# Kernel tuning notes

Measured on AMD Instinct MI355X. Metric: run time of the kernel, lower is better.

The kernel has to match this reference:

```python
import jax, jax.numpy as jnp
import numpy as np

N_NODES = 50000
N_EDGES = 800000
IN_CH = 128
HEADS = 4
HID = 32  # per-head dim; heads*hid = 128
N_GRAPHS = 128


def setup_inputs() -> dict:
    key = jax.random.key(0)
    ks = jax.random.split(key, 32)
    d = {}
    d["x"] = jax.random.normal(ks[0], (N_NODES, IN_CH), dtype=jnp.float32)
    d["edge_index"] = jax.random.randint(ks[1], (2, N_EDGES), 0, N_NODES, dtype=jnp.int64)
    d["batch"] = jnp.sort(jax.random.randint(ks[2], (N_NODES,), 0, N_GRAPHS, dtype=jnp.int64))
    HD = HEADS * HID
    names = [("wq1", (IN_CH, HD)), ("bq1", (HD,)), ("wk1", (IN_CH, HD)), ("bk1", (HD,)),
             ("wv1", (IN_CH, HD)), ("bv1", (HD,)), ("ws1", (IN_CH, HD)), ("bs1", (HD,)),
             ("wq2", (HD, HD)), ("bq2", (HD,)), ("wk2", (HD, HD)), ("bk2", (HD,)),
             ("wv2", (HD, HD)), ("bv2", (HD,)), ("ws2", (HD, HD)), ("bs2", (HD,)),
             ("wl", (HD, HD)), ("bl", (HD,)), ("wl2", (HD, 1)), ("bl2", (1,))]
    for i, (nm, shp) in enumerate(names):
        d[nm] = jax.random.normal(ks[3 + i], shp, dtype=jnp.float32) * 0.05
    return d


def _transformer_conv(x, src, dst, wq, bq, wk, bk, wv, bv, ws, bs):
    """PyG TransformerConv: multi-head dot-product attention over edges,
    softmax normalized per destination node, plus linear root/skip term."""
    N = x.shape[0]
    q = (x @ wq + bq).reshape(N, HEADS, HID)
    k = (x @ wk + bk).reshape(N, HEADS, HID)
    v = (x @ wv + bv).reshape(N, HEADS, HID)
    # edge scores: [E, H]
    e = jnp.einsum('ehd,ehd->eh', q[dst], k[src]) * np.float32(1.0 / np.sqrt(HID))
    # segment softmax over incoming edges of each destination node
    m = jax.ops.segment_max(e, dst, num_segments=N)
    a = jnp.exp(e - m[dst])
    s = jax.ops.segment_sum(a, dst, num_segments=N)
    alpha = a / s[dst]  # [E, H]
    msg = alpha[:, :, None] * v[src]  # [E, H, D]
    out = jax.ops.segment_sum(msg, dst, num_segments=N).reshape(N, HEADS * HID)
    return out + x @ ws + bs  # root weight (skip) term


def reference(x, edge_index, batch,
              wq1, bq1, wk1, bk1, wv1, bv1, ws1, bs1,
              wq2, bq2, wk2, bk2, wv2, bv2, ws2, bs2,
              wl, bl, wl2, bl2):
    src, dst = edge_index[0], edge_index[1]
    h = _transformer_conv(x, src, dst, wq1, bq1, wk1, bk1, wv1, bv1, ws1, bs1)
    h = jax.nn.relu(h)
    h = _transformer_conv(h, src, dst, wq2, bq2, wk2, bk2, wv2, bv2, ws2, bs2)
    h = jax.nn.relu(h)
    h = h @ wl + bl
    h = h @ wl2 + bl2  # [N, 1]
    # global mean pool over graphs
    sums = jax.ops.segment_sum(h, batch, num_segments=N_GRAPHS)
    cnts = jax.ops.segment_sum(jnp.ones((h.shape[0], 1), h.dtype), batch, num_segments=N_GRAPHS)
    return sums / jnp.maximum(cnts, 1.0)
```

## Files before the change

kernel.cpp:

```cpp
#include <hip/hip_runtime.h>
#include <hip/hip_bf16.h>
#include <math.h>

#define NNODES 50000
#define NEDGES 800000
#define NGRAPHS 128
#define SCAN_B ((NNODES + 255) / 256)

typedef __attribute__((ext_vector_type(8))) short bf16x8;
typedef __attribute__((ext_vector_type(4))) float f32x4;

__device__ __forceinline__ unsigned short f2bf(float f) {
    unsigned int u = __float_as_uint(f);
    return (unsigned short)((u + 0x7FFFu + ((u >> 16) & 1u)) >> 16);
}
__device__ __forceinline__ float2 bf2f2(unsigned int u) {
    float2 f;
    f.x = __uint_as_float(u << 16);
    f.y = __uint_as_float(u & 0xFFFF0000u);
    return f;
}

__global__ void count_edges(const int* __restrict__ ei, int* __restrict__ cnt) {
    int e = blockIdx.x * 256 + threadIdx.x;
    if (e < NEDGES) atomicAdd(&cnt[ei[NEDGES + e]], 1);
}

__global__ __launch_bounds__(256)
void scan_pass1(const int* __restrict__ cnt, int* __restrict__ bsum) {
    const int t = threadIdx.x;
    const int i = blockIdx.x * 256 + t;
    int v = (i < NNODES) ? cnt[i] : 0;
#pragma unroll
    for (int off = 32; off > 0; off >>= 1) v += __shfl_xor(v, off, 64);
    __shared__ int ws[4];
    if ((t & 63) == 0) ws[t >> 6] = v;
    __syncthreads();
    if (t == 0) bsum[blockIdx.x] = ws[0] + ws[1] + ws[2] + ws[3];
}

__global__ __launch_bounds__(256)
void scan_pass2(const int* __restrict__ bsum, int* __restrict__ boff) {
    const int t = threadIdx.x;
    const int v = (t < SCAN_B) ? bsum[t] : 0;
    __shared__ int a[256];
    a[t] = v;
    __syncthreads();
    for (int off = 1; off < 256; off <<= 1) {
        const int u = (t >= off) ? a[t - off] : 0;
        __syncthreads();
        a[t] += u;
        __syncthreads();
    }
    if (t < SCAN_B) boff[t] = a[t] - v;
}

__global__ __launch_bounds__(256)
void scan_pass3(const int* __restrict__ cnt, const int* __restrict__ boff,
                int* __restrict__ rowptr, int* __restrict__ wpos) {
    const int t = threadIdx.x;
    const int i = blockIdx.x * 256 + t;
    const int v = (i < NNODES) ? cnt[i] : 0;
    __shared__ int a[256];
    a[t] = v;
    __syncthreads();
    for (int off = 1; off < 256; off <<= 1) {
        const int u = (t >= off) ? a[t - off] : 0;
        __syncthreads();
        a[t] += u;
        __syncthreads();
    }
    if (i < NNODES) {
        const int e = boff[blockIdx.x] + a[t] - v;
        rowptr[i] = e;
        wpos[i]   = e;
    }
    if (i == 0) rowptr[NNODES] = NEDGES;
}

__global__ void fill_csr(const int* __restrict__ ei, int* __restrict__ wpos,
                         int* __restrict__ colsrc) {
    int e = blockIdx.x * 256 + threadIdx.x;
    if (e < NEDGES) {
        int d = ei[NEDGES + e];
        int slot = atomicAdd(&wpos[d], 1);
        colsrc[slot] = ei[e];
    }
}

__global__ void fuse_wl(const float* __restrict__ wl, const float* __restrict__ bl,
                        const float* __restrict__ wl2, const float* __restrict__ bl2,
                        float* __restrict__ wf, float* __restrict__ bf) {
    int t = threadIdx.x;
    float s = 0.f;
    for (int j = 0; j < 128; ++j) s += wl[t * 128 + j] * wl2[j];
    wf[t] = s;
    if (t == 0) {
        float s2 = 0.f;
        for (int j = 0; j < 128; ++j) s2 += bl[j] * wl2[j];
        bf[0] = s2 + bl2[0];
    }
}

__global__ void prep_w(const float* __restrict__ wq, const float* __restrict__ wk,
                       const float* __restrict__ wv, const float* __restrict__ wsk,
                       unsigned short* __restrict__ Wt) {
    const int sel = blockIdx.y;
    const float* W = sel == 0 ? wq : sel == 1 ? wk : sel == 2 ? wv : wsk;
    const int idx = blockIdx.x * 256 + threadIdx.x;
    const int col = idx & 127;
    const int k   = idx >> 7;
    Wt[sel * 16384 + col * 128 + k] = f2bf(W[k * 128 + col]);
}

__global__ __launch_bounds__(256)
void gemm_qkvs(const float* __restrict__ F, const unsigned short* __restrict__ Wt,
               const float* __restrict__ bq, const float* __restrict__ bk,
               const float* __restrict__ bv, const float* __restrict__ bsk,
               float* __restrict__ Q, unsigned short* __restrict__ Kb,
               unsigned short* __restrict__ Vb, float* __restrict__ H) {
    __shared__ __align__(16) unsigned short As[128][136];
    __shared__ __align__(16) unsigned short Bt[64][136];
    const int t    = threadIdx.x;
    const int m0   = blockIdx.x * 128;
    const int lane = t & 63;
    const int w    = t >> 6;
    const int l15  = lane & 15;
    const int lg   = lane >> 4;

    {
        const int row = t >> 1;
        const int kh  = (t & 1) * 64;
        const int gr  = min(m0 + row, NNODES - 1);
        const float* src = &F[(size_t)gr * 128 + kh];
#pragma unroll
        for (int p = 0; p < 16; ++p) {
            const float4 v = *(const float4*)&src[p * 4];
            ushort4 u;
            u.x = f2bf(v.x); u.y = f2bf(v.y); u.z = f2bf(v.z); u.w = f2bf(v.w);
            *(ushort4*)&As[row][kh + p * 4] = u;
        }
    }

    for (int sl = 0; sl < 8; ++sl) {
        const int sel = sl >> 1;
        const int c0  = (sl & 1) * 64;
        const float* bias = sel == 0 ? bq : sel == 1 ? bk : sel == 2 ? bv : bsk;

        {
            const int col = t >> 2;
            const int kb  = (t & 3) * 32;
            const unsigned short* src = &Wt[sel * 16384 + (c0 + col) * 128 + kb];
#pragma unroll
            for (int p = 0; p < 4; ++p)
                *(uint4*)&Bt[col][kb + p * 8] = *(const uint4*)&src[p * 8];
        }
        __syncthreads();

        const float b0 = bias[c0 + l15];
        const float b1 = bias[c0 + 16 + l15];
        const float b2 = bias[c0 + 32 + l15];
        const float b3 = bias[c0 + 48 + l15];
        f32x4 a00 = {b0, b0, b0, b0}, a01 = {b1, b1, b1, b1},
              a02 = {b2, b2, b2, b2}, a03 = {b3, b3, b3, b3};
        f32x4 a10 = a00, a11 = a01, a12 = a02, a13 = a03;
#pragma unroll
        for (int ks = 0; ks < 4; ++ks) {
            const int kof = ks * 32 + lg * 8;
            const bf16x8 af0 = *(const bf16x8*)&As[w * 32 + l15][kof];
            const bf16x8 af1 = *(const bf16x8*)&As[w * 32 + 16 + l15][kof];
            const bf16x8 bf0 = *(const bf16x8*)&Bt[l15][kof];
            const bf16x8 bf1 = *(const bf16x8*)&Bt[16 + l15][kof];
            const bf16x8 bf2 = *(const bf16x8*)&Bt[32 + l15][kof];
            const bf16x8 bf3 = *(const bf16x8*)&Bt[48 + l15][kof];
            a00 = __builtin_amdgcn_mfma_f32_16x16x32_bf16(af0, bf0, a00, 0, 0, 0);
            a01 = __builtin_amdgcn_mfma_f32_16x16x32_bf16(af0, bf1, a01, 0, 0, 0);
            a02 = __builtin_amdgcn_mfma_f32_16x16x32_bf16(af0, bf2, a02, 0, 0, 0);
            a03 = __builtin_amdgcn_mfma_f32_16x16x32_bf16(af0, bf3, a03, 0, 0, 0);
            a10 = __builtin_amdgcn_mfma_f32_16x16x32_bf16(af1, bf0, a10, 0, 0, 0);
            a11 = __builtin_amdgcn_mfma_f32_16x16x32_bf16(af1, bf1, a11, 0, 0, 0);
            a12 = __builtin_amdgcn_mfma_f32_16x16x32_bf16(af1, bf2, a12, 0, 0, 0);
            a13 = __builtin_amdgcn_mfma_f32_16x16x32_bf16(af1, bf3, a13, 0, 0, 0);
        }
        __syncthreads();

        const int r0 = m0 + w * 32 + lg * 4;
        if (sel == 1 || sel == 2) {
            unsigned short* Ob = sel == 1 ? Kb : Vb;
#define STB(ACC, RT, CT)                                                       \
            _Pragma("unroll")                                                  \
            for (int i = 0; i < 4; ++i) {                                      \
                const int gr = r0 + (RT) * 16 + i;                             \
                if (gr < NNODES)                                               \
                    Ob[(size_t)gr * 128 + c0 + (CT) * 16 + l15] = f2bf(ACC[i]);\
            }
            STB(a00, 0, 0) STB(a01, 0, 1) STB(a02, 0, 2) STB(a03, 0, 3)
            STB(a10, 1, 0) STB(a11, 1, 1) STB(a12, 1, 2) STB(a13, 1, 3)
#undef STB
        } else {
            float* O = sel == 0 ? Q : H;
#define ST(ACC, RT, CT)                                                        \
            _Pragma("unroll")                                                  \
            for (int i = 0; i < 4; ++i) {                                      \
                const int gr = r0 + (RT) * 16 + i;                             \
                if (gr < NNODES)                                               \
                    O[(size_t)gr * 128 + c0 + (CT) * 16 + l15] = ACC[i];       \
            }
            ST(a00, 0, 0) ST(a01, 0, 1) ST(a02, 0, 2) ST(a03, 0, 3)
            ST(a10, 1, 0) ST(a11, 1, 1) ST(a12, 1, 2) ST(a13, 1, 3)
#undef ST
        }
    }
}

template <bool FUSE_HEAD>
__global__ __launch_bounds__(128)
void attn_agg(const float* __restrict__ Q, const unsigned short* __restrict__ Kb,
              const unsigned short* __restrict__ Vb, float* __restrict__ H,
              const int* __restrict__ rowptr, const int* __restrict__ colsrc,
              const float* __restrict__ wf, float* __restrict__ r) {
    const int n    = blockIdx.x * 2 + (threadIdx.x >> 6);
    const int l    = threadIdx.x & 63;
    const int half = l >> 5;
    const int c    = (l & 31) * 4;
    const float4 q4 = *(const float4*)&Q[(size_t)n * 128 + c];
    const float sc_ = 0.17677669529663687f;
    const float q0 = q4.x * sc_, q1 = q4.y * sc_, q2 = q4.z * sc_, q3 = q4.w * sc_;
    const int beg = rowptr[n], end = rowptr[n + 1];
    const int cnt = end - beg;

    float m = -INFINITY, s = 0.f;
    float a0 = 0.f, a1 = 0.f, a2 = 0.f, a3 = 0.f;

    uint2 ku, vu;
    if (cnt > 0) {
        const int src = colsrc[min(beg + half, end - 1)];
        ku = *(const uint2*)&Kb[(size_t)src * 128 + c];
        vu = *(const uint2*)&Vb[(size_t)src * 128 + c];
    }
    for (int i = beg; i < end; i += 2) {
        const uint2 kc = ku, vc = vu;
        const bool valid = (i + half) < end;
        if (i + 2 < end) {
            const int srcN = colsrc[min(i + 2 + half, end - 1)];
            ku = *(const uint2*)&Kb[(size_t)srcN * 128 + c];
            vu = *(const uint2*)&Vb[(size_t)srcN * 128 + c];
        }
        const float2 k01 = bf2f2(kc.x), k23 = bf2f2(kc.y);
        float p = fmaf(q0, k01.x, fmaf(q1, k01.y, fmaf(q2, k23.x, q3 * k23.y)));
        p += __shfl_xor(p, 4);
        p += __shfl_xor(p, 2);
        p += __shfl_xor(p, 1);
        if (!valid) p = -INFINITY;
        const float pO = __shfl_xor(p, 32);
        const float nm = fmaxf(fmaxf(p, pO), m);
        const float sc = __expf(m - nm);
        const float w  = __expf(p - nm);
        s = fmaf(s, sc, w);
        const float2 v01 = bf2f2(vc.x), v23 = bf2f2(vc.y);
        a0 = fmaf(a0, sc, w * v01.x);
        a1 = fmaf(a1, sc, w * v01.y);
        a2 = fmaf(a2, sc, w * v23.x);
        a3 = fmaf(a3, sc, w * v23.y);
        m = nm;
    }
    s  += __shfl_xor(s, 32);
    a0 += __shfl_xor(a0, 32);
    a1 += __shfl_xor(a1, 32);
    a2 += __shfl_xor(a2, 32);
    a3 += __shfl_xor(a3, 32);

    const float4 hv = *(const float4*)&H[(size_t)n * 128 + c];
    float o0 = hv.x, o1 = hv.y, o2 = hv.z, o3 = hv.w;
    if (cnt > 0) {
        const float inv = 1.f / s;
        o0 = fmaf(a0, inv, o0);
        o1 = fmaf(a1, inv, o1);
        o2 = fmaf(a2, inv, o2);
        o3 = fmaf(a3, inv, o3);
    }
    o0 = fmaxf(o0, 0.f); o1 = fmaxf(o1, 0.f);
    o2 = fmaxf(o2, 0.f); o3 = fmaxf(o3, 0.f);
    if (!FUSE_HEAD) {
        if (half == 0) {
            float4 o; o.x = o0; o.y = o1; o.z = o2; o.w = o3;
            *(float4*)&H[(size_t)n * 128 + c] = o;
        }
    } else {
        float val = fmaf(o0, wf[c], fmaf(o1, wf[c + 1],
                    fmaf(o2, wf[c + 2], o3 * wf[c + 3])));
        val += __shfl_xor(val, 16);
        val += __shfl_xor(val, 8);
        val += __shfl_xor(val, 4);
        val += __shfl_xor(val, 2);
        val += __shfl_xor(val, 1);
        if (l == 0) r[n] = val;
    }
}

__global__ __launch_bounds__(256)
void graph_pool(const float* __restrict__ r, const int* __restrict__ batch,
                const float* __restrict__ bf, float* __restrict__ out) {
    const int g = blockIdx.x;
    const int t = threadIdx.x;
    int lo = 0, hi = NNODES;
    while (lo < hi) { int mid = (lo + hi) >> 1; if (batch[mid] < g) lo = mid + 1; else hi = mid; }
    const int beg = lo;
    lo = beg; hi = NNODES;
    while (lo < hi) { int mid = (lo + hi) >> 1; if (batch[mid] < g + 1) lo = mid + 1; else hi = mid; }
    const int end = lo;

    float s = 0.f;
    for (int i = beg + t; i < end; i += 256) s += r[i];
#pragma unroll
    for (int off = 32; off > 0; off >>= 1) s += __shfl_xor(s, off, 64);
    __shared__ float pw[4];
    if ((t & 63) == 0) pw[t >> 6] = s;
    __syncthreads();
    if (t == 0) {
        const float cnt = (float)(end - beg);
        const float tot = pw[0] + pw[1] + pw[2] + pw[3] + cnt * bf[0];
        out[g] = tot / fmaxf(cnt, 1.f);
    }
}

extern "C" void kernel_launch(void* const* d_in, const int* in_sizes, int n_in,
                              void* d_out, int out_size, void* d_ws, size_t ws_size,
                              hipStream_t stream) {
    const float* x     = (const float*)d_in[0];
    const int*   ei    = (const int*)d_in[1];
    const int*   batch = (const int*)d_in[2];
    const float* wq1 = (const float*)d_in[3];  const float* bq1 = (const float*)d_in[4];
    const float* wk1 = (const float*)d_in[5];  const float* bk1 = (const float*)d_in[6];
    const float* wv1 = (const float*)d_in[7];  const float* bv1 = (const float*)d_in[8];
    const float* ws1 = (const float*)d_in[9];  const float* bs1 = (const float*)d_in[10];
    const float* wq2 = (const float*)d_in[11]; const float* bq2 = (const float*)d_in[12];
    const float* wk2 = (const float*)d_in[13]; const float* bk2 = (const float*)d_in[14];
    const float* wv2 = (const float*)d_in[15]; const float* bv2 = (const float*)d_in[16];
    const float* ws2 = (const float*)d_in[17]; const float* bs2 = (const float*)d_in[18];
    const float* wl  = (const float*)d_in[19]; const float* bl  = (const float*)d_in[20];
    const float* wl2 = (const float*)d_in[21]; const float* bl2 = (const float*)d_in[22];

    char* wsb = (char*)d_ws;
    size_t off = 0;
    auto carve = [&](size_t bytes) -> void* {
        void* p = wsb + off;
        off = (off + bytes + 255) & ~(size_t)255;
        return p;
    };
    const size_t NM = (size_t)NNODES * 128 * sizeof(float);
    float* Q      = (float*)carve(NM);
    unsigned short* Kb = (unsigned short*)carve((size_t)NNODES * 128 * 2);
    unsigned short* Vb = (unsigned short*)carve((size_t)NNODES * 128 * 2);
    float* H1     = (float*)carve(NM);
    float* H2     = (float*)carve(NM);
    int*   rowptr = (int*)carve((NNODES + 1) * sizeof(int));
    int*   wpos   = (int*)carve(NNODES * sizeof(int));
    int*   cnt    = (int*)carve(NNODES * sizeof(int));
    int*   colsrc = (int*)carve(NEDGES * sizeof(int));
    int*   bsum   = (int*)carve(256 * sizeof(int));
    int*   boff   = (int*)carve(256 * sizeof(int));
    float* wf     = (float*)carve(129 * sizeof(float));
    float* bf     = wf + 128;
    float* nodeval = (float*)carve(NNODES * sizeof(float));
    unsigned short* Wt1 = (unsigned short*)carve(65536 * sizeof(unsigned short));
    unsigned short* Wt2 = (unsigned short*)carve(65536 * sizeof(unsigned short));

    hipMemsetAsync(cnt, 0, NNODES * sizeof(int), stream);

    count_edges<<<(NEDGES + 255) / 256, 256, 0, stream>>>(ei, cnt);
    scan_pass1<<<SCAN_B, 256, 0, stream>>>(cnt, bsum);
    scan_pass2<<<1, 256, 0, stream>>>(bsum, boff);
    scan_pass3<<<SCAN_B, 256, 0, stream>>>(cnt, boff, rowptr, wpos);
    fill_csr<<<(NEDGES + 255) / 256, 256, 0, stream>>>(ei, wpos, colsrc);
    fuse_wl<<<1, 128, 0, stream>>>(wl, bl, wl2, bl2, wf, bf);
    prep_w<<<dim3(64, 4), 256, 0, stream>>>(wq1, wk1, wv1, ws1, Wt1);
    prep_w<<<dim3(64, 4), 256, 0, stream>>>(wq2, wk2, wv2, ws2, Wt2);

    const int ggrid = (NNODES + 127) / 128;
    const int agrid = NNODES / 2;
    gemm_qkvs<<<ggrid, 256, 0, stream>>>(x, Wt1, bq1, bk1, bv1, bs1, Q, Kb, Vb, H1);
    attn_agg<false><<<agrid, 128, 0, stream>>>(Q, Kb, Vb, H1, rowptr, colsrc,
                                               nullptr, nullptr);
    gemm_qkvs<<<ggrid, 256, 0, stream>>>(H1, Wt2, bq2, bk2, bv2, bs2, Q, Kb, Vb, H2);
    attn_agg<true><<<agrid, 128, 0, stream>>>(Q, Kb, Vb, H2, rowptr, colsrc,
                                              wf, nodeval);
    graph_pool<<<NGRAPHS, 256, 0, stream>>>(nodeval, batch, bf, (float*)d_out);
}
```

Baseline: 401.6 us.

## Store Q and skip/hidden activations in bf16 and double-buffer weight tiles

Q, the skip/root term H and the layer-1 output are now kept in bf16 instead of fp32. This halves their memory traffic in the GEMM and attention kernels, and lets the second GEMM load its A operand without conversion. The GEMM also double-buffers the weight tile in shared memory, which removes one barrier per column slice, and the two prep_w launches are merged into one. The trade-off is lower precision for the query and residual values, which adds rounding error to the output.

```diff
diff --git a/kernel.cpp b/kernel.cpp
--- a/kernel.cpp
+++ b/kernel.cpp
@@ -13,6 +13,9 @@
 __device__ __forceinline__ unsigned short f2bf(float f) {
     unsigned int u = __float_as_uint(f);
     return (unsigned short)((u + 0x7FFFu + ((u >> 16) & 1u)) >> 16);
+}
+__device__ __forceinline__ unsigned pack2bf(float a, float b) {
+    return (unsigned)f2bf(a) | ((unsigned)f2bf(b) << 16);
 }
 __device__ __forceinline__ float2 bf2f2(unsigned int u) {
     float2 f;
@@ -102,25 +105,31 @@
     }
 }
 
-__global__ void prep_w(const float* __restrict__ wq, const float* __restrict__ wk,
-                       const float* __restrict__ wv, const float* __restrict__ wsk,
+__global__ void prep_w(const float* __restrict__ wq1, const float* __restrict__ wk1,
+                       const float* __restrict__ wv1, const float* __restrict__ ws1,
+                       const float* __restrict__ wq2, const float* __restrict__ wk2,
+                       const float* __restrict__ wv2, const float* __restrict__ ws2,
                        unsigned short* __restrict__ Wt) {
-    const int sel = blockIdx.y;
-    const float* W = sel == 0 ? wq : sel == 1 ? wk : sel == 2 ? wv : wsk;
+    const int layer = blockIdx.z;
+    const int sel   = blockIdx.y;
+    const float* W = layer == 0
+        ? (sel == 0 ? wq1 : sel == 1 ? wk1 : sel == 2 ? wv1 : ws1)
+        : (sel == 0 ? wq2 : sel == 1 ? wk2 : sel == 2 ? wv2 : ws2);
     const int idx = blockIdx.x * 256 + threadIdx.x;
     const int col = idx & 127;
     const int k   = idx >> 7;
-    Wt[sel * 16384 + col * 128 + k] = f2bf(W[k * 128 + col]);
-}
-
+    Wt[layer * 65536 + sel * 16384 + col * 128 + k] = f2bf(W[k * 128 + col]);
+}
+
+template <bool A_BF16>
 __global__ __launch_bounds__(256)
-void gemm_qkvs(const float* __restrict__ F, const unsigned short* __restrict__ Wt,
+void gemm_qkvs(const void* __restrict__ Fv, const unsigned short* __restrict__ Wt,
                const float* __restrict__ bq, const float* __restrict__ bk,
                const float* __restrict__ bv, const float* __restrict__ bsk,
-               float* __restrict__ Q, unsigned short* __restrict__ Kb,
-               unsigned short* __restrict__ Vb, float* __restrict__ H) {
+               unsigned short* __restrict__ Qb, unsigned short* __restrict__ Kb,
+               unsigned short* __restrict__ Vb, unsigned short* __restrict__ Hb) {
     __shared__ __align__(16) unsigned short As[128][136];
-    __shared__ __align__(16) unsigned short Bt[64][136];
+    __shared__ __align__(16) unsigned short Bt[2][64][136];
     const int t    = threadIdx.x;
     const int m0   = blockIdx.x * 128;
     const int lane = t & 63;
@@ -132,30 +141,44 @@
         const int row = t >> 1;
         const int kh  = (t & 1) * 64;
         const int gr  = min(m0 + row, NNODES - 1);
-        const float* src = &F[(size_t)gr * 128 + kh];
+        if constexpr (A_BF16) {
+            const unsigned short* src = &((const unsigned short*)Fv)[(size_t)gr * 128 + kh];
 #pragma unroll
-        for (int p = 0; p < 16; ++p) {
-            const float4 v = *(const float4*)&src[p * 4];
-            ushort4 u;
-            u.x = f2bf(v.x); u.y = f2bf(v.y); u.z = f2bf(v.z); u.w = f2bf(v.w);
-            *(ushort4*)&As[row][kh + p * 4] = u;
+            for (int p = 0; p < 8; ++p)
+                *(uint4*)&As[row][kh + p * 8] = *(const uint4*)&src[p * 8];
+        } else {
+            const float* src = &((const float*)Fv)[(size_t)gr * 128 + kh];
+#pragma unroll
+            for (int p = 0; p < 16; ++p) {
+                const float4 v = *(const float4*)&src[p * 4];
+                ushort4 u;
+                u.x = f2bf(v.x); u.y = f2bf(v.y); u.z = f2bf(v.z); u.w = f2bf(v.w);
+                *(ushort4*)&As[row][kh + p * 4] = u;
+            }
         }
     }
 
+#define STAGE_B(BUF, SL)                                                       \
+    {                                                                          \
+        const int sel_ = (SL) >> 1, c0_ = ((SL) & 1) * 64;                     \
+        const int col = t >> 2, kb = (t & 3) * 32;                             \
+        const unsigned short* src = &Wt[sel_ * 16384 + (c0_ + col) * 128 + kb];\
+        _Pragma("unroll")                                                      \
+        for (int p = 0; p < 4; ++p)                                            \
+            *(uint4*)&Bt[BUF][col][kb + p * 8] = *(const uint4*)&src[p * 8];   \
+    }
+
+    STAGE_B(0, 0)
+    __syncthreads();
+
     for (int sl = 0; sl < 8; ++sl) {
+        const int cur = sl & 1;
+        if (sl < 7) STAGE_B(cur ^ 1, sl + 1)
+
         const int sel = sl >> 1;
         const int c0  = (sl & 1) * 64;
         const float* bias = sel == 0 ? bq : sel == 1 ? bk : sel == 2 ? bv : bsk;
-
-        {
-            const int col = t >> 2;
-            const int kb  = (t & 3) * 32;
-            const unsigned short* src = &Wt[sel * 16384 + (c0 + col) * 128 + kb];
-#pragma unroll
-            for (int p = 0; p < 4; ++p)
-                *(uint4*)&Bt[col][kb + p * 8] = *(const uint4*)&src[p * 8];
-        }
-        __syncthreads();
+        unsigned short* Ob = sel == 0 ? Qb : sel == 1 ? Kb : sel == 2 ? Vb : Hb;
 
         const float b0 = bias[c0 + l15];
         const float b1 = bias[c0 + 16 + l15];
@@ -169,10 +192,10 @@
             const int kof = ks * 32 + lg * 8;
             const bf16x8 af0 = *(const bf16x8*)&As[w * 32 + l15][kof];
             const bf16x8 af1 = *(const bf16x8*)&As[w * 32 + 16 + l15][kof];
-            const bf16x8 bf0 = *(const bf16x8*)&Bt[l15][kof];
-            const bf16x8 bf1 = *(const bf16x8*)&Bt[16 + l15][kof];
-            const bf16x8 bf2 = *(const bf16x8*)&Bt[32 + l15][kof];
-            const bf16x8 bf3 = *(const bf16x8*)&Bt[48 + l15][kof];
+            const bf16x8 bf0 = *(const bf16x8*)&Bt[cur][l15][kof];
+            const bf16x8 bf1 = *(const bf16x8*)&Bt[cur][16 + l15][kof];
+            const bf16x8 bf2 = *(const bf16x8*)&Bt[cur][32 + l15][kof];
+            const bf16x8 bf3 = *(const bf16x8*)&Bt[cur][48 + l15][kof];
             a00 = __builtin_amdgcn_mfma_f32_16x16x32_bf16(af0, bf0, a00, 0, 0, 0);
             a01 = __builtin_amdgcn_mfma_f32_16x16x32_bf16(af0, bf1, a01, 0, 0, 0);
             a02 = __builtin_amdgcn_mfma_f32_16x16x32_bf16(af0, bf2, a02, 0, 0, 0);
@@ -182,50 +205,40 @@
             a12 = __builtin_amdgcn_mfma_f32_16x16x32_bf16(af1, bf2, a12, 0, 0, 0);
             a13 = __builtin_amdgcn_mfma_f32_16x16x32_bf16(af1, bf3, a13, 0, 0, 0);
         }
+
+        const int r0 = m0 + w * 32 + lg * 4;
+#define STB(ACC, RT, CT)                                                       \
+        _Pragma("unroll")                                                      \
+        for (int i = 0; i < 4; ++i) {                                          \
+            const int gr = r0 + (RT) * 16 + i;                                 \
+            if (gr < NNODES)                                                   \
+                Ob[(size_t)gr * 128 + c0 + (CT) * 16 + l15] = f2bf(ACC[i]);    \
+        }
+        STB(a00, 0, 0) STB(a01, 0, 1) STB(a02, 0, 2) STB(a03, 0, 3)
+        STB(a10, 1, 0) STB(a11, 1, 1) STB(a12, 1, 2) STB(a13, 1, 3)
+#undef STB
         __syncthreads();
-
-        const int r0 = m0 + w * 32 + lg * 4;
-        if (sel == 1 || sel == 2) {
-            unsigned short* Ob = sel == 1 ? Kb : Vb;
-#define STB(ACC, RT, CT)                                                       \
-            _Pragma("unroll")                                                  \
-            for (int i = 0; i < 4; ++i) {                                      \
-                const int gr = r0 + (RT) * 16 + i;                             \
-                if (gr < NNODES)                                               \
-                    Ob[(size_t)gr * 128 + c0 + (CT) * 16 + l15] = f2bf(ACC[i]);\
-            }
-            STB(a00, 0, 0) STB(a01, 0, 1) STB(a02, 0, 2) STB(a03, 0, 3)
-            STB(a10, 1, 0) STB(a11, 1, 1) STB(a12, 1, 2) STB(a13, 1, 3)
-#undef STB
-        } else {
-            float* O = sel == 0 ? Q : H;
-#define ST(ACC, RT, CT)                                                        \
-            _Pragma("unroll")                                                  \
-            for (int i = 0; i < 4; ++i) {                                      \
-                const int gr = r0 + (RT) * 16 + i;                             \
-                if (gr < NNODES)                                               \
-                    O[(size_t)gr * 128 + c0 + (CT) * 16 + l15] = ACC[i];       \
-            }
-            ST(a00, 0, 0) ST(a01, 0, 1) ST(a02, 0, 2) ST(a03, 0, 3)
-            ST(a10, 1, 0) ST(a11, 1, 1) ST(a12, 1, 2) ST(a13, 1, 3)
-#undef ST
-        }
-    }
+    }
+#undef STAGE_B
 }
 
 template <bool FUSE_HEAD>
 __global__ __launch_bounds__(128)
-void attn_agg(const float* __restrict__ Q, const unsigned short* __restrict__ Kb,
-              const unsigned short* __restrict__ Vb, float* __restrict__ H,
+void attn_agg(const unsigned short* __restrict__ Qb,
+              const unsigned short* __restrict__ Kb,
+              const unsigned short* __restrict__ Vb,
+              unsigned short* __restrict__ Hb,
               const int* __restrict__ rowptr, const int* __restrict__ colsrc,
               const float* __restrict__ wf, float* __restrict__ r) {
     const int n    = blockIdx.x * 2 + (threadIdx.x >> 6);
     const int l    = threadIdx.x & 63;
     const int half = l >> 5;
     const int c    = (l & 31) * 4;
-    const float4 q4 = *(const float4*)&Q[(size_t)n * 128 + c];
+    const uint2 qu = *(const uint2*)&Qb[(size_t)n * 128 + c];
+    const float2 q01 = bf2f2(qu.x), q23 = bf2f2(qu.y);
     const float sc_ = 0.17677669529663687f;
-    const float q0 = q4.x * sc_, q1 = q4.y * sc_, q2 = q4.z * sc_, q3 = q4.w * sc_;
+    const float q0 = q01.x * sc_, q1 = q01.y * sc_;
+    const float q2 = q23.x * sc_, q3 = q23.y * sc_;
     const int beg = rowptr[n], end = rowptr[n + 1];
     const int cnt = end - beg;
 
@@ -270,8 +283,9 @@
     a2 += __shfl_xor(a2, 32);
     a3 += __shfl_xor(a3, 32);
 
-    const float4 hv = *(const float4*)&H[(size_t)n * 128 + c];
-    float o0 = hv.x, o1 = hv.y, o2 = hv.z, o3 = hv.w;
+    const uint2 hu = *(const uint2*)&Hb[(size_t)n * 128 + c];
+    const float2 h01 = bf2f2(hu.x), h23 = bf2f2(hu.y);
+    float o0 = h01.x, o1 = h01.y, o2 = h23.x, o3 = h23.y;
     if (cnt > 0) {
         const float inv = 1.f / s;
         o0 = fmaf(a0, inv, o0);
@@ -283,12 +297,14 @@
     o2 = fmaxf(o2, 0.f); o3 = fmaxf(o3, 0.f);
     if (!FUSE_HEAD) {
         if (half == 0) {
-            float4 o; o.x = o0; o.y = o1; o.z = o2; o.w = o3;
-            *(float4*)&H[(size_t)n * 128 + c] = o;
+            uint2 o;
+            o.x = pack2bf(o0, o1);
+            o.y = pack2bf(o2, o3);
+            *(uint2*)&Hb[(size_t)n * 128 + c] = o;
         }
     } else {
-        float val = fmaf(o0, wf[c], fmaf(o1, wf[c + 1],
-                    fmaf(o2, wf[c + 2], o3 * wf[c + 3])));
+        const float4 w4 = *(const float4*)&wf[c];
+        float val = fmaf(o0, w4.x, fmaf(o1, w4.y, fmaf(o2, w4.z, o3 * w4.w)));
         val += __shfl_xor(val, 16);
         val += __shfl_xor(val, 8);
         val += __shfl_xor(val, 4);
@@ -348,12 +364,12 @@
         off = (off + bytes + 255) & ~(size_t)255;
         return p;
     };
-    const size_t NM = (size_t)NNODES * 128 * sizeof(float);
-    float* Q      = (float*)carve(NM);
-    unsigned short* Kb = (unsigned short*)carve((size_t)NNODES * 128 * 2);
-    unsigned short* Vb = (unsigned short*)carve((size_t)NNODES * 128 * 2);
-    float* H1     = (float*)carve(NM);
-    float* H2     = (float*)carve(NM);
+    const size_t NB = (size_t)NNODES * 128 * 2;
+    unsigned short* Qb = (unsigned short*)carve(NB);
+    unsigned short* Kb = (unsigned short*)carve(NB);
+    unsigned short* Vb = (unsigned short*)carve(NB);
+    unsigned short* H1 = (unsigned short*)carve(NB);
+    unsigned short* H2 = (unsigned short*)carve(NB);
     int*   rowptr = (int*)carve((NNODES + 1) * sizeof(int));
     int*   wpos   = (int*)carve(NNODES * sizeof(int));
     int*   cnt    = (int*)carve(NNODES * sizeof(int));
@@ -363,8 +379,7 @@
     float* wf     = (float*)carve(129 * sizeof(float));
     float* bf     = wf + 128;
     float* nodeval = (float*)carve(NNODES * sizeof(float));
-    unsigned short* Wt1 = (unsigned short*)carve(65536 * sizeof(unsigned short));
-    unsigned short* Wt2 = (unsigned short*)carve(65536 * sizeof(unsigned short));
+    unsigned short* Wt = (unsigned short*)carve(131072 * sizeof(unsigned short));
 
     hipMemsetAsync(cnt, 0, NNODES * sizeof(int), stream);
 
@@ -374,16 +389,18 @@
     scan_pass3<<<SCAN_B, 256, 0, stream>>>(cnt, boff, rowptr, wpos);
     fill_csr<<<(NEDGES + 255) / 256, 256, 0, stream>>>(ei, wpos, colsrc);
     fuse_wl<<<1, 128, 0, stream>>>(wl, bl, wl2, bl2, wf, bf);
-    prep_w<<<dim3(64, 4), 256, 0, stream>>>(wq1, wk1, wv1, ws1, Wt1);
-    prep_w<<<dim3(64, 4), 256, 0, stream>>>(wq2, wk2, wv2, ws2, Wt2);
+    prep_w<<<dim3(64, 4, 2), 256, 0, stream>>>(wq1, wk1, wv1, ws1,
+                                               wq2, wk2, wv2, ws2, Wt);
 
     const int ggrid = (NNODES + 127) / 128;
     const int agrid = NNODES / 2;
-    gemm_qkvs<<<ggrid, 256, 0, stream>>>(x, Wt1, bq1, bk1, bv1, bs1, Q, Kb, Vb, H1);
-    attn_agg<false><<<agrid, 128, 0, stream>>>(Q, Kb, Vb, H1, rowptr, colsrc,
+    gemm_qkvs<false><<<ggrid, 256, 0, stream>>>(x, Wt, bq1, bk1, bv1, bs1,
+                                                Qb, Kb, Vb, H1);
+    attn_agg<false><<<agrid, 128, 0, stream>>>(Qb, Kb, Vb, H1, rowptr, colsrc,
                                                nullptr, nullptr);
-    gemm_qkvs<<<ggrid, 256, 0, stream>>>(H1, Wt2, bq2, bk2, bv2, bs2, Q, Kb, Vb, H2);
-    attn_agg<true><<<agrid, 128, 0, stream>>>(Q, Kb, Vb, H2, rowptr, colsrc,
+    gemm_qkvs<true><<<ggrid, 256, 0, stream>>>(H1, Wt + 65536, bq2, bk2, bv2, bs2,
+                                               Qb, Kb, Vb, H2);
+    attn_agg<true><<<agrid, 128, 0, stream>>>(Qb, Kb, Vb, H2, rowptr, colsrc,
                                               wf, nodeval);
     graph_pool<<<NGRAPHS, 256, 0, stream>>>(nodeval, batch, bf, (float*)d_out);
 }
```

Result: faster. 392.8 us (-2.2%).
